# Kernel tuning notes

Hardware: AMD Instinct MI355X
Metric: run time of the kernel (lower is better)

Reference implementation:

```python
import jax, jax.numpy as jnp
import numpy as np

PADDED_NODE_ID = -1


def setup_inputs() -> dict:
    key = jax.random.key(0)
    k0, k1, k2, k3 = jax.random.split(key, 4)
    B, N, F = 1024, 512, 64
    src_ids = jax.random.randint(k0, (B, N), 0, 1000, dtype=jnp.int64 if jax.config.jax_enable_x64 else jnp.int32)
    dst_ids = jax.random.randint(k1, (B, N), 0, 1000, dtype=src_ids.dtype)
    W1 = jax.random.normal(k2, (1, F), dtype=jnp.float32) * 0.1   # Linear(1 -> F)
    b1 = jnp.zeros((F,), dtype=jnp.float32)
    W2 = jax.random.normal(k3, (F, F), dtype=jnp.float32) * 0.05  # Linear(F -> F)
    b2 = jnp.zeros((F,), dtype=jnp.float32)
    return {"src_ids": src_ids, "dst_ids": dst_ids, "W1": W1, "b1": b1, "W2": W2, "b2": b2}


def _count_freqs(src_ids, dst_ids):
    # For each row, count occurrences of each neighbor id within its own row
    # and within the paired row (cross-lookup). Equivalent to np.unique counts
    # plus dict-based cross mapping in the original, vectorized as pairwise
    # equality reductions over [B, N, N].
    def eq_count(a, b):
        return (a[:, :, None] == b[:, None, :]).sum(-1).astype(jnp.float32)  # [B, N]

    src_in_src = eq_count(src_ids, src_ids)
    src_in_dst = eq_count(src_ids, dst_ids)
    dst_in_dst = eq_count(dst_ids, dst_ids)
    dst_in_src = eq_count(dst_ids, src_ids)

    source_freq = jnp.stack([src_in_src, src_in_dst], axis=-1)  # [B, N, 2]
    dst_freq = jnp.stack([dst_in_dst, dst_in_src], axis=-1)     # [B, N, 2]

    # zero out padded positions
    source_freq = jnp.where((src_ids == PADDED_NODE_ID)[..., None], 0.0, source_freq)
    dst_freq = jnp.where((dst_ids == PADDED_NODE_ID)[..., None], 0.0, dst_freq)
    return source_freq, dst_freq


def reference(src_ids, dst_ids, W1, b1, W2, b2):
    source_freq, dst_freq = _count_freqs(src_ids, dst_ids)  # [B, N, 2] each

    def encode(freq):
        # freq[..., None] has shape [B, N, 2, 1]; Linear(1->F) is an outer product
        h = jax.nn.relu(freq[..., None] * W1[0] + b1)        # [B, N, 2, F]
        h = jnp.einsum('bnkf,fg->bnkg', h, W2) + b2          # [B, N, 2, F]
        return h.sum(axis=2)                                 # [B, N, F]

    return encode(source_freq), encode(dst_freq)
```

## Files before the change

### kernel.cpp

```cpp
#include <hip/hip_runtime.h>

#define BATCH 1024
#define NSEQ  512
#define NF    64
#define TBL_N (NSEQ + 1)
#define HIST_BINS 1024

#define HOT 32
#define TBL_BLOCKS ((TBL_N + 3) / 4)

__global__ __launch_bounds__(256) void build_table_kernel(
        const float* __restrict__ W1,
        const float* __restrict__ b1,
        const float* __restrict__ W2,
        const float* __restrict__ b2,
        float* __restrict__ tbl) {
    const int c = blockIdx.x * 4 + (threadIdx.x >> 6);
    const int g = threadIdx.x & 63;
    if (c >= TBL_N) return;
    const float cf = (float)c;
    float acc = b2[g];
#pragma unroll 8
    for (int f = 0; f < NF; ++f) {
        float h = fmaxf(cf * W1[f] + b1[f], 0.0f);
        acc += h * W2[f * NF + g];
    }
    tbl[c * NF + g] = acc;
}

__global__ __launch_bounds__(256) void expand_kernel(
        const int* __restrict__ src_ids,
        const int* __restrict__ dst_ids,
        const float* __restrict__ g_tbl,
        float* __restrict__ out) {
    __shared__ int            hist_s[HIST_BINS];
    __shared__ int            hist_d[HIST_BINS];
    __shared__ float          s_tbl[HOT * NF];
    __shared__ ushort2        s_off[NSEQ];
    __shared__ unsigned short s_ovf[NSEQ];
    __shared__ int            s_novf;

    const int t     = threadIdx.x;
    const int which = blockIdx.x & 1;
    const int row   = blockIdx.x >> 1;

    const int* __restrict__ own_ids = (which == 0) ? src_ids : dst_ids;

#pragma unroll
    for (int i = t; i < HIST_BINS; i += 256) { hist_s[i] = 0; hist_d[i] = 0; }
    if (t == 0) s_novf = 0;

    {
        const float4* __restrict__ g4 = (const float4*)g_tbl;
        float4* __restrict__ l4 = (float4*)s_tbl;
#pragma unroll
        for (int i = t; i < HOT * NF / 4; i += 256) l4[i] = g4[i];
    }
    __syncthreads();

#pragma unroll
    for (int i = t; i < NSEQ; i += 256) {
        int si = src_ids[(size_t)row * NSEQ + i];
        int di = dst_ids[(size_t)row * NSEQ + i];
        if (si >= 0) atomicAdd(&hist_s[si], 1);
        if (di >= 0) atomicAdd(&hist_d[di], 1);
    }
    __syncthreads();

#pragma unroll
    for (int i = t; i < NSEQ; i += 256) {
        int id = own_ids[(size_t)row * NSEQ + i];
        int own = 0, cross = 0;
        if (id >= 0) {
            own   = (which == 0) ? hist_s[id] : hist_d[id];
            cross = (which == 0) ? hist_d[id] : hist_s[id];
        }
        if (own >= HOT || cross >= HOT) {
            int k = atomicAdd(&s_novf, 1);
            s_ovf[k] = (unsigned short)i;
        }
        ushort2 off;
        off.x = (unsigned short)(min(own,   HOT - 1) * (NF * 4));
        off.y = (unsigned short)(min(cross, HOT - 1) * (NF * 4));
        s_off[i] = off;
    }
    __syncthreads();

    float4* __restrict__ o = (float4*)(out + ((size_t)which * BATCH + row) * NSEQ * NF);
    const char* __restrict__ tb = (const char*)s_tbl;
    const int NV = NSEQ * NF / 4;
#pragma unroll 4
    for (int e = t; e < NV; e += 256) {
        const int n  = e >> 4;
        const int fb = (e & 15) << 4;
        const ushort2 c = s_off[n];
        const float4 a0 = *(const float4*)(tb + (int)c.x + fb);
        const float4 a1 = *(const float4*)(tb + (int)c.y + fb);
        o[e] = make_float4(a0.x + a1.x, a0.y + a1.y, a0.z + a1.z, a0.w + a1.w);
    }

    __syncthreads();
    const int novf = s_novf;
    if (novf > 0) {
        const float4* __restrict__ g4 = (const float4*)g_tbl;
        for (int k = t >> 4; k < novf; k += 16) {
            const int i  = s_ovf[k];
            const int f4 = t & 15;
            const int id = own_ids[(size_t)row * NSEQ + i];
            int own = 0, cross = 0;
            if (id >= 0) {
                own   = (which == 0) ? hist_s[id] : hist_d[id];
                cross = (which == 0) ? hist_d[id] : hist_s[id];
            }
            float4 a0 = g4[own * (NF / 4) + f4];
            float4 a1 = g4[cross * (NF / 4) + f4];
            o[i * 16 + f4] = make_float4(a0.x + a1.x, a0.y + a1.y,
                                         a0.z + a1.z, a0.w + a1.w);
        }
    }
}

extern "C" void kernel_launch(void* const* d_in, const int* in_sizes, int n_in,
                              void* d_out, int out_size, void* d_ws, size_t ws_size,
                              hipStream_t stream) {
    const int*   src_ids = (const int*)d_in[0];
    const int*   dst_ids = (const int*)d_in[1];
    const float* W1 = (const float*)d_in[2];
    const float* b1 = (const float*)d_in[3];
    const float* W2 = (const float*)d_in[4];
    const float* b2 = (const float*)d_in[5];

    float* out = (float*)d_out;
    float* tbl = (float*)d_ws;

    build_table_kernel<<<TBL_BLOCKS, 256, 0, stream>>>(W1, b1, W2, b2, tbl);
    expand_kernel<<<2 * BATCH, 256, 0, stream>>>(src_ids, dst_ids, tbl, out);
}
```

Measured before the change: 50.99 us.

## Split each output row across two blocks and hoist id loads into registers

Each (which,row) is now handled by two blocks, each writing half of the 512 positions, which doubles the grid to 4096 blocks. Every block still builds both full histograms, so histogram work is duplicated. The ids are loaded into registers once at kernel start so the shared-memory table copy overlaps with them. The expand loop is fully unrolled with per-thread offsets preloaded from shared memory. The aim is more parallelism and a shorter tail, at the cost of redundant histogram construction and extra id reads.

Measured after the change: 51.62 us. Within noise of the previous version (+1.2%).

```diff
diff --git a/kernel.cpp b/kernel.cpp
--- a/kernel.cpp
+++ b/kernel.cpp
@@ -7,6 +7,7 @@
 #define HIST_BINS 1024
 
 #define HOT 32
+#define HALF 256
 #define TBL_BLOCKS ((TBL_N + 3) / 4)
 
 __global__ __launch_bounds__(256) void build_table_kernel(
@@ -36,15 +37,20 @@
     __shared__ int            hist_s[HIST_BINS];
     __shared__ int            hist_d[HIST_BINS];
     __shared__ float          s_tbl[HOT * NF];
-    __shared__ ushort2        s_off[NSEQ];
-    __shared__ unsigned short s_ovf[NSEQ];
+    __shared__ ushort2        s_off[HALF];
+    __shared__ unsigned short s_ovf[HALF];
     __shared__ int            s_novf;
 
     const int t     = threadIdx.x;
-    const int which = blockIdx.x & 1;
-    const int row   = blockIdx.x >> 1;
+    const int half  = blockIdx.x & 1;
+    const int row   = (blockIdx.x >> 1) & (BATCH - 1);
+    const int which = blockIdx.x >> 11;
 
-    const int* __restrict__ own_ids = (which == 0) ? src_ids : dst_ids;
+    const size_t rb = (size_t)row * NSEQ;
+    const int si0 = src_ids[rb + t];
+    const int si1 = src_ids[rb + t + 256];
+    const int di0 = dst_ids[rb + t];
+    const int di1 = dst_ids[rb + t + 256];
 
 #pragma unroll
     for (int i = t; i < HIST_BINS; i += 256) { hist_s[i] = 0; hist_d[i] = 0; }
@@ -58,18 +64,14 @@
     }
     __syncthreads();
 
-#pragma unroll
-    for (int i = t; i < NSEQ; i += 256) {
-        int si = src_ids[(size_t)row * NSEQ + i];
-        int di = dst_ids[(size_t)row * NSEQ + i];
-        if (si >= 0) atomicAdd(&hist_s[si], 1);
-        if (di >= 0) atomicAdd(&hist_d[di], 1);
-    }
+    if (si0 >= 0) atomicAdd(&hist_s[si0], 1);
+    if (si1 >= 0) atomicAdd(&hist_s[si1], 1);
+    if (di0 >= 0) atomicAdd(&hist_d[di0], 1);
+    if (di1 >= 0) atomicAdd(&hist_d[di1], 1);
     __syncthreads();
 
-#pragma unroll
-    for (int i = t; i < NSEQ; i += 256) {
-        int id = own_ids[(size_t)row * NSEQ + i];
+    {
+        const int id = (which == 0) ? (half ? si1 : si0) : (half ? di1 : di0);
         int own = 0, cross = 0;
         if (id >= 0) {
             own   = (which == 0) ? hist_s[id] : hist_d[id];
@@ -77,25 +79,29 @@
         }
         if (own >= HOT || cross >= HOT) {
             int k = atomicAdd(&s_novf, 1);
-            s_ovf[k] = (unsigned short)i;
+            s_ovf[k] = (unsigned short)t;
         }
         ushort2 off;
         off.x = (unsigned short)(min(own,   HOT - 1) * (NF * 4));
         off.y = (unsigned short)(min(cross, HOT - 1) * (NF * 4));
-        s_off[i] = off;
+        s_off[t] = off;
     }
     __syncthreads();
 
-    float4* __restrict__ o = (float4*)(out + ((size_t)which * BATCH + row) * NSEQ * NF);
+    float4* __restrict__ o = (float4*)(out +
+        (((size_t)which * BATCH + row) * NSEQ + (size_t)half * HALF) * NF);
     const char* __restrict__ tb = (const char*)s_tbl;
-    const int NV = NSEQ * NF / 4;
-#pragma unroll 4
-    for (int e = t; e < NV; e += 256) {
-        const int n  = e >> 4;
-        const int fb = (e & 15) << 4;
-        const ushort2 c = s_off[n];
-        const float4 a0 = *(const float4*)(tb + (int)c.x + fb);
-        const float4 a1 = *(const float4*)(tb + (int)c.y + fb);
+
+    ushort2 offs[16];
+#pragma unroll
+    for (int k = 0; k < 16; ++k) offs[k] = s_off[(t >> 4) + k * 16];
+
+    const int fb = (t & 15) << 4;
+#pragma unroll
+    for (int k = 0; k < 16; ++k) {
+        const int e = t + k * 256;
+        const float4 a0 = *(const float4*)(tb + (int)offs[k].x + fb);
+        const float4 a1 = *(const float4*)(tb + (int)offs[k].y + fb);
         o[e] = make_float4(a0.x + a1.x, a0.y + a1.y, a0.z + a1.z, a0.w + a1.w);
     }
 
@@ -106,7 +112,8 @@
         for (int k = t >> 4; k < novf; k += 16) {
             const int i  = s_ovf[k];
             const int f4 = t & 15;
-            const int id = own_ids[(size_t)row * NSEQ + i];
+            const int id = (which == 0) ? src_ids[rb + half * HALF + i]
+                                        : dst_ids[rb + half * HALF + i];
             int own = 0, cross = 0;
             if (id >= 0) {
                 own   = (which == 0) ? hist_s[id] : hist_d[id];
@@ -134,5 +141,5 @@
     float* tbl = (float*)d_ws;
 
     build_table_kernel<<<TBL_BLOCKS, 256, 0, stream>>>(W1, b1, W2, b2, tbl);
-    expand_kernel<<<2 * BATCH, 256, 0, stream>>>(src_ids, dst_ids, tbl, out);
+    expand_kernel<<<2 * 2 * BATCH, 256, 0, stream>>>(src_ids, dst_ids, tbl, out);
 }
```

## Fuse table build into expand kernel and compute overflow entries on the fly

Applied to the files above, without the earlier changes.

Removes the separate table-build launch. Each block now computes its own 16-entry hot table in shared memory, and overflow counts are computed directly from W1/b1/W2/b2 instead of read from a global table. The id loads are hoisted into registers so they are reused for both the histogram and the lookup passes. The cost is that every block redoes the small MLP for 16 rows (64 FMAs per output element), and the hot table shrinks from 32 to 16 entries, so more positions may take the slower overflow path.

Measured after the change: 54.75 us. +7.4%, slower.

```diff
diff --git a/kernel.cpp b/kernel.cpp
--- a/kernel.cpp
+++ b/kernel.cpp
@@ -3,35 +3,17 @@
 #define BATCH 1024
 #define NSEQ  512
 #define NF    64
-#define TBL_N (NSEQ + 1)
 #define HIST_BINS 1024
 
-#define HOT 32
-#define TBL_BLOCKS ((TBL_N + 3) / 4)
+#define HOT 16
 
-__global__ __launch_bounds__(256) void build_table_kernel(
+__global__ __launch_bounds__(256) void fused_kernel(
+        const int* __restrict__ src_ids,
+        const int* __restrict__ dst_ids,
         const float* __restrict__ W1,
         const float* __restrict__ b1,
         const float* __restrict__ W2,
         const float* __restrict__ b2,
-        float* __restrict__ tbl) {
-    const int c = blockIdx.x * 4 + (threadIdx.x >> 6);
-    const int g = threadIdx.x & 63;
-    if (c >= TBL_N) return;
-    const float cf = (float)c;
-    float acc = b2[g];
-#pragma unroll 8
-    for (int f = 0; f < NF; ++f) {
-        float h = fmaxf(cf * W1[f] + b1[f], 0.0f);
-        acc += h * W2[f * NF + g];
-    }
-    tbl[c * NF + g] = acc;
-}
-
-__global__ __launch_bounds__(256) void expand_kernel(
-        const int* __restrict__ src_ids,
-        const int* __restrict__ dst_ids,
-        const float* __restrict__ g_tbl,
         float* __restrict__ out) {
     __shared__ int            hist_s[HIST_BINS];
     __shared__ int            hist_d[HIST_BINS];
@@ -44,32 +26,41 @@
     const int which = blockIdx.x & 1;
     const int row   = blockIdx.x >> 1;
 
-    const int* __restrict__ own_ids = (which == 0) ? src_ids : dst_ids;
+    const size_t rb = (size_t)row * NSEQ;
+    const int si0 = src_ids[rb + t];
+    const int si1 = src_ids[rb + t + 256];
+    const int di0 = dst_ids[rb + t];
+    const int di1 = dst_ids[rb + t + 256];
 
 #pragma unroll
     for (int i = t; i < HIST_BINS; i += 256) { hist_s[i] = 0; hist_d[i] = 0; }
     if (t == 0) s_novf = 0;
 
-    {
-        const float4* __restrict__ g4 = (const float4*)g_tbl;
-        float4* __restrict__ l4 = (float4*)s_tbl;
 #pragma unroll
-        for (int i = t; i < HOT * NF / 4; i += 256) l4[i] = g4[i];
+    for (int k = 0; k < (HOT * NF) / 256; ++k) {
+        const int idx = t + k * 256;
+        const int r = idx >> 6, g = idx & 63;
+        const float cf = (float)r;
+        float acc = b2[g];
+#pragma unroll 8
+        for (int f = 0; f < NF; ++f) {
+            float h = fmaxf(cf * W1[f] + b1[f], 0.0f);
+            acc += h * W2[f * NF + g];
+        }
+        s_tbl[r * NF + g] = acc;
     }
     __syncthreads();
 
-#pragma unroll
-    for (int i = t; i < NSEQ; i += 256) {
-        int si = src_ids[(size_t)row * NSEQ + i];
-        int di = dst_ids[(size_t)row * NSEQ + i];
-        if (si >= 0) atomicAdd(&hist_s[si], 1);
-        if (di >= 0) atomicAdd(&hist_d[di], 1);
-    }
+    if (si0 >= 0) atomicAdd(&hist_s[si0], 1);
+    if (si1 >= 0) atomicAdd(&hist_s[si1], 1);
+    if (di0 >= 0) atomicAdd(&hist_d[di0], 1);
+    if (di1 >= 0) atomicAdd(&hist_d[di1], 1);
     __syncthreads();
 
 #pragma unroll
-    for (int i = t; i < NSEQ; i += 256) {
-        int id = own_ids[(size_t)row * NSEQ + i];
+    for (int u = 0; u < 2; ++u) {
+        const int i  = t + u * 256;
+        const int id = (which == 0) ? (u ? si1 : si0) : (u ? di1 : di0);
         int own = 0, cross = 0;
         if (id >= 0) {
             own   = (which == 0) ? hist_s[id] : hist_d[id];
@@ -102,20 +93,28 @@
     __syncthreads();
     const int novf = s_novf;
     if (novf > 0) {
-        const float4* __restrict__ g4 = (const float4*)g_tbl;
+        const int* __restrict__ own_ids = (which == 0) ? src_ids : dst_ids;
         for (int k = t >> 4; k < novf; k += 16) {
             const int i  = s_ovf[k];
             const int f4 = t & 15;
-            const int id = own_ids[(size_t)row * NSEQ + i];
+            const int g0 = f4 * 4;
+            const int id = own_ids[rb + i];
             int own = 0, cross = 0;
             if (id >= 0) {
                 own   = (which == 0) ? hist_s[id] : hist_d[id];
                 cross = (which == 0) ? hist_d[id] : hist_s[id];
             }
-            float4 a0 = g4[own * (NF / 4) + f4];
-            float4 a1 = g4[cross * (NF / 4) + f4];
-            o[i * 16 + f4] = make_float4(a0.x + a1.x, a0.y + a1.y,
-                                         a0.z + a1.z, a0.w + a1.w);
+            float a0 = 2.0f * b2[g0 + 0], a1 = 2.0f * b2[g0 + 1];
+            float a2 = 2.0f * b2[g0 + 2], a3 = 2.0f * b2[g0 + 3];
+            for (int f = 0; f < NF; ++f) {
+                float w = W1[f], b = b1[f];
+                float hs = fmaxf((float)own * w + b, 0.0f)
+                         + fmaxf((float)cross * w + b, 0.0f);
+                const float* w2 = &W2[f * NF + g0];
+                a0 += hs * w2[0]; a1 += hs * w2[1];
+                a2 += hs * w2[2]; a3 += hs * w2[3];
+            }
+            o[i * 16 + f4] = make_float4(a0, a1, a2, a3);
         }
     }
 }
@@ -131,8 +130,7 @@
     const float* b2 = (const float*)d_in[5];
 
     float* out = (float*)d_out;
-    float* tbl = (float*)d_ws;
 
-    build_table_kernel<<<TBL_BLOCKS, 256, 0, stream>>>(W1, b1, W2, b2, tbl);
-    expand_kernel<<<2 * BATCH, 256, 0, stream>>>(src_ids, dst_ids, tbl, out);
+    fused_kernel<<<2 * BATCH, 256, 0, stream>>>(src_ids, dst_ids,
+                                                W1, b1, W2, b2, out);
 }
```
